# Kernel tuning notes

Hardware: AMD Instinct MI355X
Metric: run time of the kernel (lower is better)

Reference implementation:

```python
import jax, jax.numpy as jnp
import numpy as np

N_NODES = 100000
N_EDGES = 1600000
IN_DIM = 128
HID = 128
OUT_DIM = 2
NUM_GRAPHS = 64
BN_EPS = 1e-5


def _glorot(key, shape):
    fan_in, fan_out = shape[0], shape[1]
    lim = np.sqrt(6.0 / (fan_in + fan_out))
    return jax.random.uniform(key, shape, jnp.float32, -lim, lim)


def setup_inputs() -> dict:
    key = jax.random.key(0)
    ks = jax.random.split(key, 12)
    x = jax.random.normal(ks[0], (N_NODES, IN_DIM), jnp.float32)
    edge_index = jax.random.randint(ks[1], (2, N_EDGES), 0, N_NODES, jnp.int64)
    batch = jnp.sort(jax.random.randint(ks[2], (N_NODES,), 0, NUM_GRAPHS, jnp.int64))
    return {
        "x": x,
        "edge_index": edge_index,
        "batch": batch,
        "W1": _glorot(ks[3], (IN_DIM, HID)), "b1": jnp.zeros((HID,), jnp.float32),
        "g1": jnp.ones((HID,), jnp.float32), "be1": jnp.zeros((HID,), jnp.float32),
        "W2": _glorot(ks[4], (HID, HID)), "b2": jnp.zeros((HID,), jnp.float32),
        "g2": jnp.ones((HID,), jnp.float32), "be2": jnp.zeros((HID,), jnp.float32),
        "Wc1": _glorot(ks[5], (HID, HID // 2)), "bc1": jnp.zeros((HID // 2,), jnp.float32),
        "Wc2": _glorot(ks[6], (HID // 2, OUT_DIM)), "bc2": jnp.zeros((OUT_DIM,), jnp.float32),
    }


def gcn_conv(x, src, dst, W, b):
    # PyG GCNConv: add self-loops, symmetric deg^{-1/2} normalization
    n = x.shape[0]
    loop = jnp.arange(n, dtype=src.dtype)
    s = jnp.concatenate([src, loop])
    d = jnp.concatenate([dst, loop])
    deg = jax.ops.segment_sum(jnp.ones_like(d, dtype=x.dtype), d, num_segments=n)
    dinv = jnp.where(deg > 0, jax.lax.rsqrt(deg), 0.0)
    xw = x @ W  # [N, out]
    msgs = xw[s] * (dinv[s] * dinv[d])[:, None]  # [E+N, out]
    out = jax.ops.segment_sum(msgs, d, num_segments=n)
    return out + b


def batchnorm(x, gamma, beta):
    mean = jnp.mean(x, axis=0)
    var = jnp.mean(jnp.square(x - mean), axis=0)  # biased, as torch BN
    return (x - mean) * jax.lax.rsqrt(var + BN_EPS) * gamma + beta


def reference(x, edge_index, batch, W1, b1, g1, be1, W2, b2, g2, be2, Wc1, bc1, Wc2, bc2):
    src, dst = edge_index[0], edge_index[1]
    x = jnp.nan_to_num(x, nan=0.0)
    # layer 1: GCNConv -> BN -> ReLU (dropout = identity in eval)
    h = jax.nn.relu(batchnorm(gcn_conv(x, src, dst, W1, b1), g1, be1))
    # layer 2
    h = jax.nn.relu(batchnorm(gcn_conv(h, src, dst, W2, b2), g2, be2))
    # global mean pool per graph
    sums = jax.ops.segment_sum(h, batch, num_segments=NUM_GRAPHS)
    counts = jax.ops.segment_sum(jnp.ones((h.shape[0],), h.dtype), batch, num_segments=NUM_GRAPHS)
    pooled = sums / jnp.maximum(counts, 1.0)[:, None]  # [G, HID]
    # classifier MLP
    z = jax.nn.relu(pooled @ Wc1 + bc1)
    out = z @ Wc2 + bc2
    return jnp.nan_to_num(out, nan=0.0)
```

## Files before the change

### kernel.cpp

```cpp
#include <hip/hip_runtime.h>

typedef unsigned int uint;
typedef unsigned short ushort;

#define HID 128
#define NGRAPH 64

typedef __attribute__((ext_vector_type(8))) short short8;
typedef __attribute__((ext_vector_type(4))) float floatx4;

__device__ __forceinline__ float bflo(uint w){ return __uint_as_float(w<<16); }
__device__ __forceinline__ float bfhi(uint w){ return __uint_as_float(w & 0xffff0000u); }
__device__ __forceinline__ float bf2f(ushort u){ return __uint_as_float(((uint)u)<<16); }
__device__ __forceinline__ ushort f2bf(float f){
  uint u = __float_as_uint(f);
  u = u + 0x7fffu + ((u>>16)&1u);
  return (ushort)(u>>16);
}
__device__ __forceinline__ uint pack2(float a, float b){
  return (uint)f2bf(a) | ((uint)f2bf(b)<<16);
}
__device__ __forceinline__ float nanz(float v){ return (v==v) ? v : 0.f; }

__device__ __forceinline__ int esrc(const int* ei, int e, int E, int is64){
  return is64 ? ei[2*(size_t)e] : ei[e];
}
__device__ __forceinline__ int edst(const int* ei, int e, int E, int is64){
  return is64 ? ei[2*((size_t)E + e)] : ei[E + e];
}
__device__ __forceinline__ int bat(const int* b, int i, int is64){
  return is64 ? b[2*(size_t)i] : b[i];
}

__global__ void k_detect(const int* __restrict__ ei, int* __restrict__ flags){
  __shared__ int h2;
  if (threadIdx.x == 0) h2 = 0;
  __syncthreads();
  int t = threadIdx.x;
  if (t < 128){ if (ei[2*t + 1] != 0) atomicAdd(&h2, 1); }
  __syncthreads();
  if (t == 0) flags[1] = (h2 == 0) ? 1 : 0;
}

__global__ void k_sentinel(ushort* out, int n){
  int i = blockIdx.x*blockDim.x + threadIdx.x;
  if (i < n) out[i] = 0x429A;
}

__global__ void k_wprep(const float* __restrict__ W1, const float* __restrict__ W2,
                        ushort* __restrict__ wt1, ushort* __restrict__ wt2){
  const float* W  = (blockIdx.x == 0) ? W1  : W2;
  ushort*      Wt = (blockIdx.x == 0) ? wt1 : wt2;
  for (int o = threadIdx.x; o < 16384; o += 256){
    int j    = o & 7;
    int lane = (o >> 3) & 63;
    int ct   = (o >> 9) & 7;
    int ks   = o >> 12;
    int k = ks*32 + (lane >> 4)*8 + j;
    int n = ct*16 + (lane & 15);
    Wt[o] = f2bf(W[(size_t)k*HID + n]);
  }
}


__global__ void k_hist(const int* __restrict__ ei, int* __restrict__ cnt, int E, int NN,
                       const int* __restrict__ flags){
  int is64 = flags[1];
  int e = blockIdx.x*blockDim.x + threadIdx.x;
  if (e < E){ int d = edst(ei, e, E, is64); if ((uint)d < (uint)NN) atomicAdd(&cnt[d], 1); }
}

__global__ void k_scan1(const int* __restrict__ cnt, int* __restrict__ partials,
                        float* __restrict__ dinv, int NN){
  int t = threadIdx.x;
  int base = blockIdx.x*1024 + t*4;
  int v0=0,v1=0,v2=0,v3=0;
  if (base + 3 < NN){ int4 v = *(const int4*)(cnt + base); v0=v.x; v1=v.y; v2=v.z; v3=v.w; }
  else {
    if (base+0 < NN) v0 = cnt[base+0];
    if (base+1 < NN) v1 = cnt[base+1];
    if (base+2 < NN) v2 = cnt[base+2];
    if (base+3 < NN) v3 = cnt[base+3];
  }
  if (base+0 < NN) dinv[base+0] = rsqrtf((float)(v0+1));
  if (base+1 < NN) dinv[base+1] = rsqrtf((float)(v1+1));
  if (base+2 < NN) dinv[base+2] = rsqrtf((float)(v2+1));
  if (base+3 < NN) dinv[base+3] = rsqrtf((float)(v3+1));
  __shared__ int red[256];
  red[t] = v0+v1+v2+v3;
  __syncthreads();
  for (int off=128; off>0; off>>=1){
    if (t < off) red[t] += red[t+off];
    __syncthreads();
  }
  if (t==0) partials[blockIdx.x] = red[0];
}

__global__ void k_scan2(int* __restrict__ partials, int* __restrict__ offs, int npart, int NN){
  if (threadIdx.x==0 && blockIdx.x==0){
    int run = 0;
    for (int i=0;i<npart;i++){ int tt = partials[i]; partials[i] = run; run += tt; }
    offs[NN] = run;
  }
}

__global__ void k_scan3(const int* __restrict__ cnt, const int* __restrict__ partials,
                        int* __restrict__ offs, int NN){
  int t = threadIdx.x;
  int base = blockIdx.x*1024 + t*4;
  int v0=0,v1=0,v2=0,v3=0;
  if (base + 3 < NN){ int4 v = *(const int4*)(cnt + base); v0=v.x; v1=v.y; v2=v.z; v3=v.w; }
  else {
    if (base+0 < NN) v0 = cnt[base+0];
    if (base+1 < NN) v1 = cnt[base+1];
    if (base+2 < NN) v2 = cnt[base+2];
    if (base+3 < NN) v3 = cnt[base+3];
  }
  int tsum = v0+v1+v2+v3;
  __shared__ int sc[256];
  sc[t] = tsum;
  __syncthreads();
  for (int off=1; off<256; off<<=1){
    int val = (t >= off) ? sc[t-off] : 0;
    __syncthreads();
    sc[t] += val;
    __syncthreads();
  }
  int run = partials[blockIdx.x] + sc[t] - tsum;
  if (base+0 < NN){ offs[base+0] = run; run += v0; }
  if (base+1 < NN){ offs[base+1] = run; run += v1; }
  if (base+2 < NN){ offs[base+2] = run; run += v2; }
  if (base+3 < NN){ offs[base+3] = run; run += v3; }
}

__global__ void k_scatter(const int* __restrict__ ei, const int* __restrict__ offs,
                          int* __restrict__ cursor, int* __restrict__ srclist, int E, int NN,
                          const int* __restrict__ flags){
  int is64 = flags[1];
  int e = blockIdx.x*blockDim.x + threadIdx.x;
  if (e < E){
    int d = edst(ei, e, E, is64), s = esrc(ei, e, E, is64);
    if ((uint)d < (uint)NN && (uint)s < (uint)NN){
      int p = offs[d] + atomicAdd(&cursor[d], 1);
      srclist[p] = s;
    }
  }
}


__global__ __launch_bounds__(256) void k_gemm1(const float* __restrict__ A,
    const ushort* __restrict__ Wt, const float* __restrict__ dinv,
    ushort* __restrict__ O, int NN){
  __shared__ ushort wlds[16384];
  int tid = threadIdx.x;
  {
    const uint4* s = (const uint4*)Wt;
    uint4* d = (uint4*)wlds;
    #pragma unroll
    for (int i = 0; i < 8; i++) d[tid + i*256] = s[tid + i*256];
  }
  __syncthreads();
  int wave = tid >> 6, lane = tid & 63, m = lane & 15, q = lane >> 4;
  int rowbase = blockIdx.x*64 + wave*16;
  int ar = rowbase + m; if (ar >= NN) ar = NN-1;
  const float* arow = A + (size_t)ar*HID;
  short8 af[4];
  #pragma unroll
  for (int ks=0; ks<4; ks++){
    int kb = ks*32 + q*8;
    float4 f0 = *(const float4*)(arow + kb);
    float4 f1 = *(const float4*)(arow + kb + 4);
    short8 t;
    t[0]=(short)f2bf(nanz(f0.x)); t[1]=(short)f2bf(nanz(f0.y));
    t[2]=(short)f2bf(nanz(f0.z)); t[3]=(short)f2bf(nanz(f0.w));
    t[4]=(short)f2bf(nanz(f1.x)); t[5]=(short)f2bf(nanz(f1.y));
    t[6]=(short)f2bf(nanz(f1.z)); t[7]=(short)f2bf(nanz(f1.w));
    af[ks] = t;
  }
  floatx4 acc[8];
  #pragma unroll
  for (int ct=0; ct<8; ct++) acc[ct] = (floatx4){0.f,0.f,0.f,0.f};
  #pragma unroll
  for (int ks=0; ks<4; ks++){
    #pragma unroll
    for (int ct=0; ct<8; ct++){
      short8 bfrag = *(const short8*)&wlds[(((ks*8+ct)*64) + lane)*8];
      acc[ct] = __builtin_amdgcn_mfma_f32_16x16x32_bf16(af[ks], bfrag, acc[ct], 0, 0, 0);
    }
  }
  float dv[4];
  #pragma unroll
  for (int i=0;i<4;i++){ int r = rowbase + q*4 + i; dv[i] = (r < NN) ? dinv[r] : 0.f; }
  #pragma unroll
  for (int ct=0; ct<8; ct++){
    #pragma unroll
    for (int i=0;i<4;i++){
      int r = rowbase + q*4 + i;
      if (r < NN) O[(size_t)r*HID + ct*16 + m] = f2bf(acc[ct][i]*dv[i]);
    }
  }
}


__global__ __launch_bounds__(256) void k_gemm2(const uint* __restrict__ agg,
    const float* __restrict__ coef, const ushort* __restrict__ Wt,
    const float* __restrict__ dinv, ushort* __restrict__ O, int NN){
  __shared__ ushort wlds[16384];
  __shared__ float cA[128], cB[128];
  int tid = threadIdx.x;
  {
    const uint4* s = (const uint4*)Wt;
    uint4* d = (uint4*)wlds;
    #pragma unroll
    for (int i = 0; i < 8; i++) d[tid + i*256] = s[tid + i*256];
    if (tid < 128){ cA[tid] = coef[tid]; cB[tid] = coef[128+tid]; }
  }
  __syncthreads();
  int wave = tid >> 6, lane = tid & 63, m = lane & 15, q = lane >> 4;
  int rowbase = blockIdx.x*64 + wave*16;
  int ar = rowbase + m; if (ar >= NN) ar = NN-1;
  const uint* arow = agg + (size_t)ar*64;
  short8 af[4];
  #pragma unroll
  for (int ks=0; ks<4; ks++){
    int kb = ks*32 + q*8;
    uint4 u = *(const uint4*)(arow + (kb >> 1));
    short8 t;
    uint uw[4] = {u.x, u.y, u.z, u.w};
    #pragma unroll
    for (int p=0; p<4; p++){
      int k0 = kb + 2*p;
      float v0 = fmaxf(cA[k0]  *bflo(uw[p]) + cB[k0],   0.f);
      float v1 = fmaxf(cA[k0+1]*bfhi(uw[p]) + cB[k0+1], 0.f);
      t[2*p]   = (short)f2bf(v0);
      t[2*p+1] = (short)f2bf(v1);
    }
    af[ks] = t;
  }
  floatx4 acc[8];
  #pragma unroll
  for (int ct=0; ct<8; ct++) acc[ct] = (floatx4){0.f,0.f,0.f,0.f};
  #pragma unroll
  for (int ks=0; ks<4; ks++){
    #pragma unroll
    for (int ct=0; ct<8; ct++){
      short8 bfrag = *(const short8*)&wlds[(((ks*8+ct)*64) + lane)*8];
      acc[ct] = __builtin_amdgcn_mfma_f32_16x16x32_bf16(af[ks], bfrag, acc[ct], 0, 0, 0);
    }
  }
  float dv[4];
  #pragma unroll
  for (int i=0;i<4;i++){ int r = rowbase + q*4 + i; dv[i] = (r < NN) ? dinv[r] : 0.f; }
  #pragma unroll
  for (int ct=0; ct<8; ct++){
    #pragma unroll
    for (int i=0;i<4;i++){
      int r = rowbase + q*4 + i;
      if (r < NN) O[(size_t)r*HID + ct*16 + m] = f2bf(acc[ct][i]*dv[i]);
    }
  }
}


__global__ __launch_bounds__(256) void k_agg(const uint* __restrict__ xw,
    const int* __restrict__ offs, const int* __restrict__ srclist,
    const float* __restrict__ dinv, uint* __restrict__ agg,
    float* __restrict__ stats, int NN){
  __shared__ float lstat[256];
  lstat[threadIdx.x] = 0.f;
  __syncthreads();
  int wib = threadIdx.x >> 6;
  int lane = threadIdx.x & 63;
  int wid = blockIdx.x*4 + wib;
  int nw = gridDim.x*4;
  float s0=0.f, s1=0.f, q0=0.f, q1=0.f;
  for (int n = wid; n < NN; n += nw){
    int lo = offs[n], hi = offs[n+1];
    float dvn = dinv[n];
    float a0 = 0.f, a1 = 0.f;
    for (int base = lo; base < hi; base += 64){
      int c = hi - base; if (c > 64) c = 64;
      int sidx = (lane < c) ? srclist[base + lane] : 0;
      int ng = (c + 7) >> 3;
      for (int g = 0; g < ng; g++){
        int jb = g*8;
        uint w[8];
        #pragma unroll
        for (int t = 0; t < 8; t++){
          int sj = __shfl(sidx, jb + t, 64);
          w[t] = xw[(size_t)sj*64 + lane];
        }
        #pragma unroll
        for (int t = 0; t < 8; t++){
          uint wv = (jb + t < c) ? w[t] : 0u;
          a0 += bflo(wv);
          a1 += bfhi(wv);
        }
      }
    }
    uint wsf = xw[(size_t)n*64 + lane];
    a0 = (a0 + bflo(wsf)) * dvn;
    a1 = (a1 + bfhi(wsf)) * dvn;
    agg[(size_t)n*64 + lane] = pack2(a0, a1);
    s0 += a0; s1 += a1; q0 += a0*a0; q1 += a1*a1;
  }
  int ch = lane*2;
  atomicAdd(&lstat[ch],       s0);
  atomicAdd(&lstat[ch+1],     s1);
  atomicAdd(&lstat[128+ch],   q0);
  atomicAdd(&lstat[128+ch+1], q1);
  __syncthreads();
  atomicAdd(&stats[threadIdx.x], lstat[threadIdx.x]);
}


__global__ void k_bnfin(float* __restrict__ stats, const float* __restrict__ gam,
                        const float* __restrict__ bet, float* __restrict__ coef, int NN){
  int t = threadIdx.x;
  float s = stats[t], sq = stats[128+t];
  float inv = 1.f/(float)NN;
  float mean = s*inv;
  float var = fmaxf(sq*inv - mean*mean, 0.f);
  float a = gam[t] * rsqrtf(var + 1e-5f);
  coef[t] = a;
  coef[128+t] = bet[t] - mean*a;
  stats[t] = 0.f; stats[128+t] = 0.f;
}


#define PSPLIT 16

__global__ __launch_bounds__(256) void k_pool(const uint* __restrict__ agg32,
    const int* __restrict__ batch, const float* __restrict__ coef,
    float* __restrict__ pooled, int* __restrict__ counts,
    int NN, const int* __restrict__ flags){
  int is64 = flags[1];
  __shared__ int bounds[2];
  int g  = blockIdx.x;
  int si = blockIdx.y;
  if (threadIdx.x == 0){
    int lo=0, hi=NN;
    while (lo<hi){ int mid=(lo+hi)>>1; if (bat(batch,mid,is64) < g) lo=mid+1; else hi=mid; }
    bounds[0] = lo;
    int lo2=lo, hi2=NN;
    while (lo2<hi2){ int mid=(lo2+hi2)>>1; if (bat(batch,mid,is64) < g+1) lo2=mid+1; else hi2=mid; }
    bounds[1] = lo2;
    if (si == 0) counts[g] = hi2 - lo;
  }
  __syncthreads();
  int lo = bounds[0], hi = bounds[1];
  int cnt = hi - lo;
  int chunk = (cnt + PSPLIT - 1) / PSPLIT;
  int s = lo + si*chunk;
  int e = s + chunk; if (e > hi) e = hi;
  int tid = threadIdx.x;
  int lane = tid & 63, rg = tid >> 6;
  int ch = lane*2;
  float a0c = coef[ch],   b0c = coef[128+ch];
  float a1c = coef[ch+1], b1c = coef[128+ch+1];
  float acc0 = 0.f, acc1 = 0.f;
  for (int r = s + rg; r < e; r += 4){
    uint w = agg32[(size_t)r*64 + lane];
    acc0 += fmaxf(a0c*bflo(w) + b0c, 0.f);
    acc1 += fmaxf(a1c*bfhi(w) + b1c, 0.f);
  }
  __shared__ float red[512];
  red[tid] = acc0;
  red[256+tid] = acc1;
  __syncthreads();
  if (tid < 64){
    float s0 = red[tid] + red[tid+64] + red[tid+128] + red[tid+192];
    float s1 = red[256+tid] + red[320+tid] + red[384+tid] + red[448+tid];
    atomicAdd(&pooled[g*HID + ch],     s0);
    atomicAdd(&pooled[g*HID + ch + 1], s1);
  }
}


__global__ void k_mlp(const float* __restrict__ pooled, const int* __restrict__ counts,
                      const float* __restrict__ Wc1, const float* __restrict__ bc1,
                      const float* __restrict__ Wc2, const float* __restrict__ bc2,
                      float* __restrict__ out){
  __shared__ float P[NGRAPH*HID];
  __shared__ float Z[NGRAPH*64];
  int tid = threadIdx.x;
  for (int i = tid; i < NGRAPH*HID; i += 256){
    int g = i >> 7;
    float c = (float)counts[g];
    P[i] = pooled[i] / fmaxf(c, 1.f);
  }
  __syncthreads();
  for (int idx = tid; idx < NGRAPH*64; idx += 256){
    int g = idx >> 6, j = idx & 63;
    float acc = bc1[j];
    for (int k = 0; k < HID; k++) acc += P[g*HID + k] * Wc1[k*64 + j];
    Z[idx] = fmaxf(acc, 0.f);
  }
  __syncthreads();
  if (tid < NGRAPH*2){
    int g = tid >> 1, o = tid & 1;
    float acc = bc2[o];
    for (int k = 0; k < 64; k++) acc += Z[g*64 + k] * Wc2[k*2 + o];
    out[tid] = nanz(acc);
  }
}

extern "C" void kernel_launch(void* const* d_in, const int* in_sizes, int n_in,
                              void* d_out, int out_size, void* d_ws, size_t ws_size,
                              hipStream_t stream){
  const float* x   = (const float*)d_in[0];
  const int*   ei  = (const int*)d_in[1];
  const int* batch = (const int*)d_in[2];
  const float* W1  = (const float*)d_in[3];
  const float* g1  = (const float*)d_in[5];
  const float* be1 = (const float*)d_in[6];
  const float* W2  = (const float*)d_in[7];
  const float* g2  = (const float*)d_in[9];
  const float* be2 = (const float*)d_in[10];
  const float* Wc1 = (const float*)d_in[11];
  const float* bc1 = (const float*)d_in[12];
  const float* Wc2 = (const float*)d_in[13];
  const float* bc2 = (const float*)d_in[14];

  const int NN = in_sizes[2];
  const int E  = in_sizes[1] / 2;

  char* p = (char*)d_ws;
  auto carve = [&](size_t bytes)->char*{
    char* r = p; p += (bytes + 255) & ~(size_t)255; return r;
  };
  int NPART = (NN + 1023)/1024;
  int*   flags    = (int*)  carve(64*4);
  int*   cnt      = (int*)  carve((size_t)NN*4);
  int*   cursor   = (int*)  carve((size_t)NN*4);
  int*   offs     = (int*)  carve(((size_t)NN+1)*4);
  int*   partials = (int*)  carve((size_t)NPART*4);
  int*   srclist  = (int*)  carve((size_t)E*4);
  float* dinv     = (float*)carve((size_t)NN*4);
  float* stats    = (float*)carve(256*4);
  float* coef     = (float*)carve(256*4);
  float* pooled   = (float*)carve((size_t)NGRAPH*HID*4);
  int*   counts   = (int*)  carve(NGRAPH*4);
  ushort* wt1     = (ushort*)carve(16384*2);
  ushort* wt2     = (ushort*)carve(16384*2);
  ushort* xw      = (ushort*)carve((size_t)NN*HID*2);
  ushort* agg     = (ushort*)carve((size_t)NN*HID*2);
  if ((size_t)(p - (char*)d_ws) > ws_size){
    k_sentinel<<<(out_size+255)/256, 256, 0, stream>>>((ushort*)d_out, out_size);
    return;
  }

  hipMemsetAsync(cnt,    0, (size_t)NN*4, stream);
  hipMemsetAsync(cursor, 0, (size_t)NN*4, stream);
  hipMemsetAsync(stats,  0, 256*4, stream);
  hipMemsetAsync(pooled, 0, (size_t)NGRAPH*HID*4, stream);

  k_detect <<<1, 256, 0, stream>>>(ei, flags);
  k_wprep  <<<2, 256, 0, stream>>>(W1, W2, wt1, wt2);

  int eb = (E + 255)/256;
  k_hist   <<<eb, 256, 0, stream>>>(ei, cnt, E, NN, flags);
  k_scan1  <<<NPART, 256, 0, stream>>>(cnt, partials, dinv, NN);
  k_scan2  <<<1, 64, 0, stream>>>(partials, offs, NPART, NN);
  k_scan3  <<<NPART, 256, 0, stream>>>(cnt, partials, offs, NN);
  k_scatter<<<eb, 256, 0, stream>>>(ei, offs, cursor, srclist, E, NN, flags);

  int gblocks = (NN + 63)/64;
  k_gemm1<<<gblocks, 256, 0, stream>>>(x, wt1, dinv, xw, NN);
  k_agg  <<<2048, 256, 0, stream>>>((const uint*)xw, offs, srclist, dinv, (uint*)agg, stats, NN);
  k_bnfin<<<1, 128, 0, stream>>>(stats, g1, be1, coef, NN);
  k_gemm2<<<gblocks, 256, 0, stream>>>((const uint*)agg, coef, wt2, dinv, xw, NN);
  k_agg  <<<2048, 256, 0, stream>>>((const uint*)xw, offs, srclist, dinv, (uint*)agg, stats, NN);
  k_bnfin<<<1, 128, 0, stream>>>(stats, g2, be2, coef, NN);
  k_pool <<<dim3(NGRAPH, PSPLIT), 256, 0, stream>>>((const uint*)agg, batch, coef, pooled, counts, NN, flags);
  k_mlp  <<<1, 256, 0, stream>>>(pooled, counts, Wc1, bc1, Wc2, bc2, (float*)d_out);
}
```

Measured before the change: 609.8 us.

## Restructure aggregation gather with 16B loads, fuse BN finalize and memsets

Rewrites the edge-aggregation kernel so each wave gathers two neighbor rows per step with 16-byte loads (16 lanes per row) and reduces across lane groups, padding with a zero row instead of masking. The separate BN-finalize kernels are folded into the consumers (gemm2 and pool), memsets and the dtype-detect kernel are merged into one zero kernel, and the scan now writes absolute cursors so the scatter no longer reads offsets. The aim is to cut gather instruction count and launch overhead. In exchange, the per-node cross-lane reductions and more shared-memory atomics for the statistics add some cost.

```diff
diff --git a/kernel.cpp b/kernel.cpp
--- a/kernel.cpp
+++ b/kernel.cpp
@@ -22,24 +22,25 @@
 }
 __device__ __forceinline__ float nanz(float v){ return (v==v) ? v : 0.f; }
 
-__device__ __forceinline__ int esrc(const int* ei, int e, int E, int is64){
-  return is64 ? ei[2*(size_t)e] : ei[e];
-}
-__device__ __forceinline__ int edst(const int* ei, int e, int E, int is64){
-  return is64 ? ei[2*((size_t)E + e)] : ei[E + e];
-}
 __device__ __forceinline__ int bat(const int* b, int i, int is64){
   return is64 ? b[2*(size_t)i] : b[i];
 }
 
-__global__ void k_detect(const int* __restrict__ ei, int* __restrict__ flags){
-  __shared__ int h2;
-  if (threadIdx.x == 0) h2 = 0;
-  __syncthreads();
-  int t = threadIdx.x;
-  if (t < 128){ if (ei[2*t + 1] != 0) atomicAdd(&h2, 1); }
-  __syncthreads();
-  if (t == 0) flags[1] = (h2 == 0) ? 1 : 0;
+__global__ void k_zero(int* __restrict__ cnt, float* __restrict__ stats1,
+                       float* __restrict__ stats2, float* __restrict__ pooled,
+                       uint* __restrict__ xwzero, int NN,
+                       const int* __restrict__ ei, int* __restrict__ flags){
+  int i = blockIdx.x*blockDim.x + threadIdx.x;
+  for (int t = i; t < NN; t += gridDim.x*blockDim.x) cnt[t] = 0;
+  if (i < 256){ stats1[i] = 0.f; stats2[i] = 0.f; }
+  if (i < NGRAPH*HID) pooled[i] = 0.f;
+  if (i < 64) xwzero[i] = 0u;
+  if (blockIdx.x == 0 && threadIdx.x < 64){
+    int t = threadIdx.x;
+    bool nz = (ei[2*t + 1] != 0) || (ei[2*(t+64) + 1] != 0);
+    unsigned long long m = __ballot(nz);
+    if (t == 0) flags[1] = (m == 0ULL) ? 1 : 0;
+  }
 }
 
 __global__ void k_sentinel(ushort* out, int n){
@@ -67,7 +68,10 @@
                        const int* __restrict__ flags){
   int is64 = flags[1];
   int e = blockIdx.x*blockDim.x + threadIdx.x;
-  if (e < E){ int d = edst(ei, e, E, is64); if ((uint)d < (uint)NN) atomicAdd(&cnt[d], 1); }
+  if (e < E){
+    int d = is64 ? ((const int2*)ei)[(size_t)E + e].x : ei[E + e];
+    if ((uint)d < (uint)NN) atomicAdd(&cnt[d], 1);
+  }
 }
 
 __global__ void k_scan1(const int* __restrict__ cnt, int* __restrict__ partials,
@@ -105,7 +109,7 @@
 }
 
 __global__ void k_scan3(const int* __restrict__ cnt, const int* __restrict__ partials,
-                        int* __restrict__ offs, int NN){
+                        int* __restrict__ offs, int* __restrict__ cursor, int NN){
   int t = threadIdx.x;
   int base = blockIdx.x*1024 + t*4;
   int v0=0,v1=0,v2=0,v3=0;
@@ -127,21 +131,28 @@
     __syncthreads();
   }
   int run = partials[blockIdx.x] + sc[t] - tsum;
-  if (base+0 < NN){ offs[base+0] = run; run += v0; }
-  if (base+1 < NN){ offs[base+1] = run; run += v1; }
-  if (base+2 < NN){ offs[base+2] = run; run += v2; }
-  if (base+3 < NN){ offs[base+3] = run; run += v3; }
-}
-
-__global__ void k_scatter(const int* __restrict__ ei, const int* __restrict__ offs,
-                          int* __restrict__ cursor, int* __restrict__ srclist, int E, int NN,
+  if (base+0 < NN){ offs[base+0] = run; cursor[base+0] = run; run += v0; }
+  if (base+1 < NN){ offs[base+1] = run; cursor[base+1] = run; run += v1; }
+  if (base+2 < NN){ offs[base+2] = run; cursor[base+2] = run; run += v2; }
+  if (base+3 < NN){ offs[base+3] = run; cursor[base+3] = run; run += v3; }
+}
+
+__global__ void k_scatter(const int* __restrict__ ei, int* __restrict__ cursor,
+                          int* __restrict__ srclist, int E, int NN,
                           const int* __restrict__ flags){
   int is64 = flags[1];
   int e = blockIdx.x*blockDim.x + threadIdx.x;
   if (e < E){
-    int d = edst(ei, e, E, is64), s = esrc(ei, e, E, is64);
+    int d, s;
+    if (is64){
+      d = ((const int2*)ei)[(size_t)E + e].x;
+      s = ((const int2*)ei)[e].x;
+    } else {
+      d = ei[E + e];
+      s = ei[e];
+    }
     if ((uint)d < (uint)NN && (uint)s < (uint)NN){
-      int p = offs[d] + atomicAdd(&cursor[d], 1);
+      int p = atomicAdd(&cursor[d], 1);
       srclist[p] = s;
     }
   }
@@ -203,8 +214,9 @@
 
 
 __global__ __launch_bounds__(256) void k_gemm2(const uint* __restrict__ agg,
-    const float* __restrict__ coef, const ushort* __restrict__ Wt,
-    const float* __restrict__ dinv, ushort* __restrict__ O, int NN){
+    const float* __restrict__ stats, const float* __restrict__ gam,
+    const float* __restrict__ bet, const ushort* __restrict__ Wt,
+    const float* __restrict__ dinv, ushort* __restrict__ O, int NN, float invn){
   __shared__ ushort wlds[16384];
   __shared__ float cA[128], cB[128];
   int tid = threadIdx.x;
@@ -213,7 +225,14 @@
     uint4* d = (uint4*)wlds;
     #pragma unroll
     for (int i = 0; i < 8; i++) d[tid + i*256] = s[tid + i*256];
-    if (tid < 128){ cA[tid] = coef[tid]; cB[tid] = coef[128+tid]; }
+    if (tid < 128){
+      float sm = stats[tid], sq = stats[128+tid];
+      float mean = sm*invn;
+      float var = fmaxf(sq*invn - mean*mean, 0.f);
+      float a = gam[tid] * rsqrtf(var + 1e-5f);
+      cA[tid] = a;
+      cB[tid] = bet[tid] - mean*a;
+    }
   }
   __syncthreads();
   int wave = tid >> 6, lane = tid & 63, m = lane & 15, q = lane >> 4;
@@ -271,74 +290,95 @@
   __syncthreads();
   int wib = threadIdx.x >> 6;
   int lane = threadIdx.x & 63;
+  int g = lane >> 4;
+  int coloff = (lane & 15)*4;
   int wid = blockIdx.x*4 + wib;
   int nw = gridDim.x*4;
-  float s0=0.f, s1=0.f, q0=0.f, q1=0.f;
   for (int n = wid; n < NN; n += nw){
     int lo = offs[n], hi = offs[n+1];
     float dvn = dinv[n];
-    float a0 = 0.f, a1 = 0.f;
+    float acc[8];
+    #pragma unroll
+    for (int t=0;t<8;t++) acc[t]=0.f;
     for (int base = lo; base < hi; base += 64){
       int c = hi - base; if (c > 64) c = 64;
-      int sidx = (lane < c) ? srclist[base + lane] : 0;
-      int ng = (c + 7) >> 3;
-      for (int g = 0; g < ng; g++){
-        int jb = g*8;
-        uint w[8];
+      int sidx = (lane < c) ? srclist[base + lane] : NN;
+      int nst = (c + 7) >> 3;
+      for (int st = 0; st < nst; st++){
+        int j = st*8;
+        int sa = __shfl(sidx, j + g, 64);
+        int sb = __shfl(sidx, j + 4 + g, 64);
+        uint4 wa = *(const uint4*)(xw + (size_t)sa*64 + coloff);
+        uint4 wb = *(const uint4*)(xw + (size_t)sb*64 + coloff);
+        uint ua[4] = {wa.x, wa.y, wa.z, wa.w};
+        uint ub[4] = {wb.x, wb.y, wb.z, wb.w};
         #pragma unroll
-        for (int t = 0; t < 8; t++){
-          int sj = __shfl(sidx, jb + t, 64);
-          w[t] = xw[(size_t)sj*64 + lane];
+        for (int p=0;p<4;p++){
+          acc[2*p]   += bflo(ua[p]);
+          acc[2*p+1] += bfhi(ua[p]);
         }
         #pragma unroll
-        for (int t = 0; t < 8; t++){
-          uint wv = (jb + t < c) ? w[t] : 0u;
-          a0 += bflo(wv);
-          a1 += bfhi(wv);
+        for (int p=0;p<4;p++){
+          acc[2*p]   += bflo(ub[p]);
+          acc[2*p+1] += bfhi(ub[p]);
         }
       }
     }
-    uint wsf = xw[(size_t)n*64 + lane];
-    a0 = (a0 + bflo(wsf)) * dvn;
-    a1 = (a1 + bfhi(wsf)) * dvn;
-    agg[(size_t)n*64 + lane] = pack2(a0, a1);
-    s0 += a0; s1 += a1; q0 += a0*a0; q1 += a1*a1;
-  }
-  int ch = lane*2;
-  atomicAdd(&lstat[ch],       s0);
-  atomicAdd(&lstat[ch+1],     s1);
-  atomicAdd(&lstat[128+ch],   q0);
-  atomicAdd(&lstat[128+ch+1], q1);
+    #pragma unroll
+    for (int t=0;t<8;t++){
+      acc[t] += __shfl_xor(acc[t], 16, 64);
+      acc[t] += __shfl_xor(acc[t], 32, 64);
+    }
+    if (g == 0){
+      uint4 ws = *(const uint4*)(xw + (size_t)n*64 + coloff);
+      uint us[4] = {ws.x, ws.y, ws.z, ws.w};
+      float a[8];
+      #pragma unroll
+      for (int p=0;p<4;p++){
+        a[2*p]   = (acc[2*p]   + bflo(us[p])) * dvn;
+        a[2*p+1] = (acc[2*p+1] + bfhi(us[p])) * dvn;
+      }
+      uint4 o;
+      o.x = pack2(a[0],a[1]);
+      o.y = pack2(a[2],a[3]);
+      o.z = pack2(a[4],a[5]);
+      o.w = pack2(a[6],a[7]);
+      *(uint4*)(agg + (size_t)n*64 + coloff) = o;
+      #pragma unroll
+      for (int t=0;t<8;t++){
+        int ch = coloff*2 + t;
+        atomicAdd(&lstat[ch],     a[t]);
+        atomicAdd(&lstat[128+ch], a[t]*a[t]);
+      }
+    }
+  }
   __syncthreads();
   atomicAdd(&stats[threadIdx.x], lstat[threadIdx.x]);
 }
 
 
-__global__ void k_bnfin(float* __restrict__ stats, const float* __restrict__ gam,
-                        const float* __restrict__ bet, float* __restrict__ coef, int NN){
-  int t = threadIdx.x;
-  float s = stats[t], sq = stats[128+t];
-  float inv = 1.f/(float)NN;
-  float mean = s*inv;
-  float var = fmaxf(sq*inv - mean*mean, 0.f);
-  float a = gam[t] * rsqrtf(var + 1e-5f);
-  coef[t] = a;
-  coef[128+t] = bet[t] - mean*a;
-  stats[t] = 0.f; stats[128+t] = 0.f;
-}
-
-
 #define PSPLIT 16
 
 __global__ __launch_bounds__(256) void k_pool(const uint* __restrict__ agg32,
-    const int* __restrict__ batch, const float* __restrict__ coef,
+    const int* __restrict__ batch, const float* __restrict__ stats,
+    const float* __restrict__ gam, const float* __restrict__ bet,
     float* __restrict__ pooled, int* __restrict__ counts,
-    int NN, const int* __restrict__ flags){
+    int NN, const int* __restrict__ flags, float invn){
   int is64 = flags[1];
   __shared__ int bounds[2];
+  __shared__ float cA[128], cB[128];
   int g  = blockIdx.x;
   int si = blockIdx.y;
-  if (threadIdx.x == 0){
+  int tid = threadIdx.x;
+  if (tid < 128){
+    float sm = stats[tid], sq = stats[128+tid];
+    float mean = sm*invn;
+    float var = fmaxf(sq*invn - mean*mean, 0.f);
+    float a = gam[tid] * rsqrtf(var + 1e-5f);
+    cA[tid] = a;
+    cB[tid] = bet[tid] - mean*a;
+  }
+  if (tid == 0){
     int lo=0, hi=NN;
     while (lo<hi){ int mid=(lo+hi)>>1; if (bat(batch,mid,is64) < g) lo=mid+1; else hi=mid; }
     bounds[0] = lo;
@@ -353,11 +393,10 @@
   int chunk = (cnt + PSPLIT - 1) / PSPLIT;
   int s = lo + si*chunk;
   int e = s + chunk; if (e > hi) e = hi;
-  int tid = threadIdx.x;
   int lane = tid & 63, rg = tid >> 6;
   int ch = lane*2;
-  float a0c = coef[ch],   b0c = coef[128+ch];
-  float a1c = coef[ch+1], b1c = coef[128+ch+1];
+  float a0c = cA[ch],   b0c = cB[ch];
+  float a1c = cA[ch+1], b1c = cB[ch+1];
   float acc0 = 0.f, acc1 = 0.f;
   for (int r = s + rg; r < e; r += 4){
     uint w = agg32[(size_t)r*64 + lane];
@@ -432,46 +471,43 @@
   int NPART = (NN + 1023)/1024;
   int*   flags    = (int*)  carve(64*4);
   int*   cnt      = (int*)  carve((size_t)NN*4);
-  int*   cursor   = (int*)  carve((size_t)NN*4);
+  int*   cursor   = (int*)  carve(((size_t)NN+1)*4);
   int*   offs     = (int*)  carve(((size_t)NN+1)*4);
   int*   partials = (int*)  carve((size_t)NPART*4);
   int*   srclist  = (int*)  carve((size_t)E*4);
   float* dinv     = (float*)carve((size_t)NN*4);
-  float* stats    = (float*)carve(256*4);
-  float* coef     = (float*)carve(256*4);
+  float* stats1   = (float*)carve(256*4);
+  float* stats2   = (float*)carve(256*4);
   float* pooled   = (float*)carve((size_t)NGRAPH*HID*4);
   int*   counts   = (int*)  carve(NGRAPH*4);
   ushort* wt1     = (ushort*)carve(16384*2);
   ushort* wt2     = (ushort*)carve(16384*2);
-  ushort* xw      = (ushort*)carve((size_t)NN*HID*2);
+  ushort* xw      = (ushort*)carve(((size_t)NN+1)*HID*2);
   ushort* agg     = (ushort*)carve((size_t)NN*HID*2);
   if ((size_t)(p - (char*)d_ws) > ws_size){
     k_sentinel<<<(out_size+255)/256, 256, 0, stream>>>((ushort*)d_out, out_size);
     return;
   }
 
-  hipMemsetAsync(cnt,    0, (size_t)NN*4, stream);
-  hipMemsetAsync(cursor, 0, (size_t)NN*4, stream);
-  hipMemsetAsync(stats,  0, 256*4, stream);
-  hipMemsetAsync(pooled, 0, (size_t)NGRAPH*HID*4, stream);
-
-  k_detect <<<1, 256, 0, stream>>>(ei, flags);
-  k_wprep  <<<2, 256, 0, stream>>>(W1, W2, wt1, wt2);
+  const float invn = 1.f/(float)NN;
+
+  k_zero <<<512, 256, 0, stream>>>(cnt, stats1, stats2, pooled,
+                                   (uint*)(xw + (size_t)NN*HID), NN, ei, flags);
+  k_wprep<<<2, 256, 0, stream>>>(W1, W2, wt1, wt2);
 
   int eb = (E + 255)/256;
   k_hist   <<<eb, 256, 0, stream>>>(ei, cnt, E, NN, flags);
   k_scan1  <<<NPART, 256, 0, stream>>>(cnt, partials, dinv, NN);
   k_scan2  <<<1, 64, 0, stream>>>(partials, offs, NPART, NN);
-  k_scan3  <<<NPART, 256, 0, stream>>>(cnt, partials, offs, NN);
-  k_scatter<<<eb, 256, 0, stream>>>(ei, offs, cursor, srclist, E, NN, flags);
+  k_scan3  <<<NPART, 256, 0, stream>>>(cnt, partials, offs, cursor, NN);
+  k_scatter<<<eb, 256, 0, stream>>>(ei, cursor, srclist, E, NN, flags);
 
   int gblocks = (NN + 63)/64;
   k_gemm1<<<gblocks, 256, 0, stream>>>(x, wt1, dinv, xw, NN);
-  k_agg  <<<2048, 256, 0, stream>>>((const uint*)xw, offs, srclist, dinv, (uint*)agg, stats, NN);
-  k_bnfin<<<1, 128, 0, stream>>>(stats, g1, be1, coef, NN);
-  k_gemm2<<<gblocks, 256, 0, stream>>>((const uint*)agg, coef, wt2, dinv, xw, NN);
-  k_agg  <<<2048, 256, 0, stream>>>((const uint*)xw, offs, srclist, dinv, (uint*)agg, stats, NN);
-  k_bnfin<<<1, 128, 0, stream>>>(stats, g2, be2, coef, NN);
-  k_pool <<<dim3(NGRAPH, PSPLIT), 256, 0, stream>>>((const uint*)agg, batch, coef, pooled, counts, NN, flags);
+  k_agg  <<<2048, 256, 0, stream>>>((const uint*)xw, offs, srclist, dinv, (uint*)agg, stats1, NN);
+  k_gemm2<<<gblocks, 256, 0, stream>>>((const uint*)agg, stats1, g1, be1, wt2, dinv, xw, NN, invn);
+  k_agg  <<<2048, 256, 0, stream>>>((const uint*)xw, offs, srclist, dinv, (uint*)agg, stats2, NN);
+  k_pool <<<dim3(NGRAPH, PSPLIT), 256, 0, stream>>>((const uint*)agg, batch, stats2, g2, be2,
+                                                    pooled, counts, NN, flags, invn);
   k_mlp  <<<1, 256, 0, stream>>>(pooled, counts, Wc1, bc1, Wc2, bc2, (float*)d_out);
 }
```

New measurement: 737.1 us. 1.21x slower.
